# Performance work log

Hardware: AMD Instinct MI355X
Metric: run time of the kernel (lower is better)

Reference implementation:

```python
import jax, jax.numpy as jnp
import numpy as np

VOCAB, EMB, OUT = 32000, 1024, 10
B, S = 64, 512

def setup_inputs() -> dict:
    key = jax.random.key(0)
    k1, k2, k3, k4, k5, k6, k7 = jax.random.split(key, 7)
    x = jax.random.randint(k1, (B, S), 0, VOCAB)
    label = jax.random.randint(k2, (B,), 0, OUT)
    emb_table = jax.random.normal(k3, (VOCAB, EMB), dtype=jnp.float32) * 0.02
    W = jax.random.normal(k4, (EMB, EMB), dtype=jnp.float32) / np.sqrt(EMB)
    b = jax.random.normal(k5, (EMB,), dtype=jnp.float32) * 0.01
    Wc = jax.random.normal(k6, (OUT, EMB), dtype=jnp.float32) / np.sqrt(EMB)
    bc = jax.random.normal(k7, (OUT,), dtype=jnp.float32) * 0.01
    return {"x": x, "label": label, "emb_table": emb_table, "W": W, "b": b, "Wc": Wc, "bc": bc}

def reference(x, label, emb_table, W, b, Wc, bc):
    # embedding lookup: (B, S, EMB)
    emb = emb_table[x]
    # affine recurrence h_i = W @ (h_{i-1} + x_i) + b, h_{-1} = 0
    def step(h, xi):
        h = (h + xi) @ W.T + b  # (B, EMB)
        return h, h
    h0 = jnp.zeros((emb.shape[0], emb.shape[2]), dtype=emb.dtype)
    _, hs = jax.lax.scan(step, h0, jnp.swapaxes(emb, 0, 1))  # hs: (S, B, EMB)
    result = jnp.swapaxes(hs, 0, 1)  # (B, S, EMB)
    pred = result @ Wc.T + bc  # (B, S, OUT)
    pred_mean = jnp.mean(pred, axis=1)  # (B, OUT)
    # cross entropy (mean reduction)
    logp = jax.nn.log_softmax(pred_mean, axis=-1)
    loss = -jnp.mean(jnp.take_along_axis(logp, label[:, None], axis=-1))
    return loss
```

## Files before the change

### kernel.cpp

```cpp
#include <hip/hip_runtime.h>

#define OFF_C    0L
#define OFF_CS   11272192L
#define OFF_WP   11354112L
#define OFF_BS   11436032L
#define OFF_PRED 11446272L
#define OFF_PART 11446912L
#define OFF_U16  11774592L
#define UQAH 0L
#define UQAL 1048576L
#define UQATH 2097152L
#define UQATL 3145728L
#define UQBH 4194304L
#define UQBL 5242880L
#define UQBTH 6291456L
#define UQBTL 7340032L
#define URH  8388608L
#define CSA  1409024L
#define CSB  2621440L

typedef unsigned short u16;
typedef unsigned int u32;
typedef u16 us8 __attribute__((ext_vector_type(8)));
typedef short s8v __attribute__((ext_vector_type(8)));
typedef float f4v __attribute__((ext_vector_type(4)));

__device__ __forceinline__ u16 f2b(float f) {
    u32 u = __float_as_uint(f);
    return (u16)((u + 0x7fffu + ((u >> 16) & 1u)) >> 16);
}
__device__ __forceinline__ float b2f(u16 h) {
    return __uint_as_float((u32)h << 16);
}

__global__ __launch_bounds__(256) void split_w(
    const float* __restrict__ W, u16* __restrict__ Qh, u16* __restrict__ Ql,
    u16* __restrict__ QTh, u16* __restrict__ QTl)
{
    __shared__ u32 T[64][65];
    const int tid = threadIdx.x;
    const int r = tid >> 2, c0 = (tid & 3) << 4;
    alignas(16) u16 h[16], l[16];
    const size_t src = (size_t)(blockIdx.y * 64 + r) * 1024 + blockIdx.x * 64 + c0;
    #pragma unroll
    for (int q = 0; q < 4; q++) {
        float4 v = *(const float4*)(W + src + q * 4);
        float vv[4] = {v.x, v.y, v.z, v.w};
        #pragma unroll
        for (int i = 0; i < 4; i++) {
            u16 hh = f2b(vv[i]);
            u16 ll = f2b(vv[i] - b2f(hh));
            h[q * 4 + i] = hh; l[q * 4 + i] = ll;
            T[c0 + q * 4 + i][r] = ((u32)ll << 16) | hh;
        }
    }
    *(us8*)(Qh + src) = *(const us8*)&h[0];
    *(us8*)(Qh + src + 8) = *(const us8*)&h[8];
    *(us8*)(Ql + src) = *(const us8*)&l[0];
    *(us8*)(Ql + src + 8) = *(const us8*)&l[8];
    __syncthreads();
    alignas(16) u16 th[16], tl[16];
    #pragma unroll
    for (int i = 0; i < 16; i++) {
        u32 v = T[r][c0 + i];
        th[i] = (u16)(v & 0xffffu); tl[i] = (u16)(v >> 16);
    }
    const size_t dst = (size_t)(blockIdx.x * 64 + r) * 1024 + blockIdx.y * 64 + c0;
    *(us8*)(QTh + dst) = *(const us8*)&th[0];
    *(us8*)(QTh + dst + 8) = *(const us8*)&th[8];
    *(us8*)(QTl + dst) = *(const us8*)&tl[0];
    *(us8*)(QTl + dst + 8) = *(const us8*)&tl[8];
}

__global__ __launch_bounds__(256) void thin_d0(
    const float* __restrict__ Wc, const float* __restrict__ W, float* __restrict__ pbuf)
{
    const int o = blockIdx.x >> 2;
    const int d = ((blockIdx.x & 3) << 8) + threadIdx.x;
    const int k0 = blockIdx.y << 7;
    float acc = 0.f;
    #pragma unroll 8
    for (int k = k0; k < k0 + 128; k++)
        acc = fmaf(Wc[o * 1024 + k], W[(size_t)k * 1024 + d], acc);
    pbuf[(size_t)blockIdx.y * 10240 + o * 1024 + d] = acc;
}

__global__ __launch_bounds__(256) void d0_fin(
    const float* __restrict__ pbuf, u16* __restrict__ Rh)
{
    const int od = blockIdx.x * 256 + threadIdx.x;
    float v = 0.f;
    #pragma unroll
    for (int z = 0; z < 8; z++) v += pbuf[(size_t)z * 10240 + od];
    Rh[od] = f2b(v);
}

__global__ __launch_bounds__(256) void gemm_mfma(
    const u16* __restrict__ Ah_g, const u16* __restrict__ Al_g,
    const u16* __restrict__ Rh_g,
    const u16* __restrict__ BTh_g, const u16* __restrict__ BTl_g,
    float* __restrict__ C, int a1M, int a2M, int kc, long cS)
{
    const int M = a1M + a2M;
    __shared__ alignas(16) u16 Ash[4][129][8], Asl[4][129][8];
    __shared__ alignas(16) u16 Bsh[4][129][8], Bsl[4][129][8];
    const int tid = threadIdx.x;
    const int bn = blockIdx.x << 7, bm = blockIdx.y << 7;
    const int kstart = blockIdx.z * kc, kend = kstart + kc;
    const int lane = tid & 63, wid = tid >> 6;
    const int wm = (wid & 1) << 6, wn = (wid >> 1) << 6;
    const int lrow = lane & 15, kq = lane >> 4;
    const int srow = tid >> 1;
    const int skq = (tid & 1) << 1;
    const int sk = skq << 3;

    const u16* pBh = BTh_g + (size_t)(bn + srow) * 1024;
    const u16* pBl = BTl_g + (size_t)(bn + srow) * 1024;

    f4v acc[4][4];
    #pragma unroll
    for (int i = 0; i < 4; i++)
        #pragma unroll
        for (int j = 0; j < 4; j++) acc[i][j] = 0.f;

    if (bm < a1M) {
        const u16* pAh = Ah_g + (size_t)(bm + srow) * 1024;
        const u16* pAl = Al_g + (size_t)(bm + srow) * 1024;
        us8 ah0, ah1, al0, al1, bh0, bh1, bl0, bl1;
        auto loadstep = [&](int k) {
            ah0 = *(const us8*)(pAh + k + sk); ah1 = *(const us8*)(pAh + k + sk + 8);
            al0 = *(const us8*)(pAl + k + sk); al1 = *(const us8*)(pAl + k + sk + 8);
            bh0 = *(const us8*)(pBh + k + sk); bh1 = *(const us8*)(pBh + k + sk + 8);
            bl0 = *(const us8*)(pBl + k + sk); bl1 = *(const us8*)(pBl + k + sk + 8);
        };
        loadstep(kstart);
        for (int k0 = kstart; k0 < kend; k0 += 32) {
            *(us8*)&Ash[skq][srow][0] = ah0;
            *(us8*)&Ash[skq + 1][srow][0] = ah1;
            *(us8*)&Asl[skq][srow][0] = al0;
            *(us8*)&Asl[skq + 1][srow][0] = al1;
            *(us8*)&Bsh[skq][srow][0] = bh0;
            *(us8*)&Bsh[skq + 1][srow][0] = bh1;
            *(us8*)&Bsl[skq][srow][0] = bl0;
            *(us8*)&Bsl[skq + 1][srow][0] = bl1;
            __syncthreads();
            if (k0 + 32 < kend) loadstep(k0 + 32);
            s8v afh[4], afl[4], bfh[4], bfl[4];
            #pragma unroll
            for (int i = 0; i < 4; i++) {
                afh[i] = *(const s8v*)&Ash[kq][wm + (i << 4) + lrow][0];
                afl[i] = *(const s8v*)&Asl[kq][wm + (i << 4) + lrow][0];
                bfh[i] = *(const s8v*)&Bsh[kq][wn + (i << 4) + lrow][0];
                bfl[i] = *(const s8v*)&Bsl[kq][wn + (i << 4) + lrow][0];
            }
            #pragma unroll
            for (int mi = 0; mi < 4; mi++)
                #pragma unroll
                for (int ni = 0; ni < 4; ni++) {
                    acc[mi][ni] = __builtin_amdgcn_mfma_f32_16x16x32_bf16(
                        afh[mi], bfh[ni], acc[mi][ni], 0, 0, 0);
                    acc[mi][ni] = __builtin_amdgcn_mfma_f32_16x16x32_bf16(
                        afl[mi], bfh[ni], acc[mi][ni], 0, 0, 0);
                    acc[mi][ni] = __builtin_amdgcn_mfma_f32_16x16x32_bf16(
                        afh[mi], bfl[ni], acc[mi][ni], 0, 0, 0);
                }
            __syncthreads();
        }
    } else {
        const int rr = bm + srow - a1M;
        const bool aval = (rr < a2M);
        const u16* pAh = Rh_g + (size_t)(aval ? rr : 0) * 1024;
        us8 ah0, ah1, bh0, bh1, bl0, bl1;
        auto loadstep = [&](int k) {
            if (aval) {
                ah0 = *(const us8*)(pAh + k + sk); ah1 = *(const us8*)(pAh + k + sk + 8);
            } else { ah0 = 0; ah1 = 0; }
            bh0 = *(const us8*)(pBh + k + sk); bh1 = *(const us8*)(pBh + k + sk + 8);
            bl0 = *(const us8*)(pBl + k + sk); bl1 = *(const us8*)(pBl + k + sk + 8);
        };
        loadstep(kstart);
        for (int k0 = kstart; k0 < kend; k0 += 32) {
            *(us8*)&Ash[skq][srow][0] = ah0;
            *(us8*)&Ash[skq + 1][srow][0] = ah1;
            *(us8*)&Bsh[skq][srow][0] = bh0;
            *(us8*)&Bsh[skq + 1][srow][0] = bh1;
            *(us8*)&Bsl[skq][srow][0] = bl0;
            *(us8*)&Bsl[skq + 1][srow][0] = bl1;
            __syncthreads();
            if (k0 + 32 < kend) loadstep(k0 + 32);
            s8v afh[4], bfh[4], bfl[4];
            #pragma unroll
            for (int i = 0; i < 4; i++) {
                afh[i] = *(const s8v*)&Ash[kq][wm + (i << 4) + lrow][0];
                bfh[i] = *(const s8v*)&Bsh[kq][wn + (i << 4) + lrow][0];
                bfl[i] = *(const s8v*)&Bsl[kq][wn + (i << 4) + lrow][0];
            }
            #pragma unroll
            for (int mi = 0; mi < 4; mi++)
                #pragma unroll
                for (int ni = 0; ni < 4; ni++) {
                    acc[mi][ni] = __builtin_amdgcn_mfma_f32_16x16x32_bf16(
                        afh[mi], bfh[ni], acc[mi][ni], 0, 0, 0);
                    acc[mi][ni] = __builtin_amdgcn_mfma_f32_16x16x32_bf16(
                        afh[mi], bfl[ni], acc[mi][ni], 0, 0, 0);
                }
            __syncthreads();
        }
    }
    float* Cz = C + (size_t)blockIdx.z * cS;
    #pragma unroll
    for (int mi = 0; mi < 4; mi++)
        #pragma unroll
        for (int i = 0; i < 4; i++) {
            const int gr = bm + wm + (mi << 4) + (kq << 2) + i;
            if (gr >= M) continue;
            #pragma unroll
            for (int ni = 0; ni < 4; ni++)
                Cz[(size_t)gr * 1024 + bn + wn + (ni << 4) + lrow] = acc[mi][ni][i];
        }
}

__global__ __launch_bounds__(256) void combine(
    const float* __restrict__ C, int zsplit, long cS, int a1M, int a2M, int M,
    u16* __restrict__ Qh, u16* __restrict__ Ql,
    u16* __restrict__ QTh, u16* __restrict__ QTl,
    u16* __restrict__ Rh)
{
    __shared__ u32 T[64][65];
    const int tid = threadIdx.x;
    const int r = tid >> 2, c0 = (tid & 3) << 4;
    const int row0 = blockIdx.y << 6, col0 = blockIdx.x << 6;
    const int gr = row0 + r;
    const bool isQ = (row0 < a1M);
    alignas(16) u16 h[16], l[16];
    #pragma unroll
    for (int q = 0; q < 4; q++) {
        float4 v = make_float4(0.f, 0.f, 0.f, 0.f);
        if (gr < M) {
            const float* p = C + (size_t)gr * 1024 + col0 + c0 + q * 4;
            v = *(const float4*)p;
            for (int z = 1; z < zsplit; z++) {
                float4 t = *(const float4*)(p + (size_t)z * cS);
                v.x += t.x; v.y += t.y; v.z += t.z; v.w += t.w;
            }
        }
        float vv[4] = {v.x, v.y, v.z, v.w};
        #pragma unroll
        for (int i = 0; i < 4; i++) {
            u16 hh = f2b(vv[i]);
            u16 ll = f2b(vv[i] - b2f(hh));
            h[q * 4 + i] = hh; l[q * 4 + i] = ll;
            if (isQ) T[c0 + q * 4 + i][r] = ((u32)ll << 16) | hh;
        }
    }
    if (isQ) {
        const size_t dst = (size_t)gr * 1024 + col0 + c0;
        *(us8*)(Qh + dst) = *(const us8*)&h[0];
        *(us8*)(Qh + dst + 8) = *(const us8*)&h[8];
        *(us8*)(Ql + dst) = *(const us8*)&l[0];
        *(us8*)(Ql + dst + 8) = *(const us8*)&l[8];
        __syncthreads();
        alignas(16) u16 th[16], tl[16];
        #pragma unroll
        for (int i = 0; i < 16; i++) {
            u32 v = T[r][c0 + i];
            th[i] = (u16)(v & 0xffffu); tl[i] = (u16)(v >> 16);
        }
        const size_t dt = (size_t)(col0 + r) * 1024 + row0 + c0;
        *(us8*)(QTh + dt) = *(const us8*)&th[0];
        *(us8*)(QTh + dt + 8) = *(const us8*)&th[8];
        *(us8*)(QTl + dt) = *(const us8*)&tl[0];
        *(us8*)(QTl + dt + 8) = *(const us8*)&tl[8];
    } else if (gr < M) {
        const size_t dst = (size_t)(gr - a1M + a2M) * 1024 + col0 + c0;
        *(us8*)(Rh + dst) = *(const us8*)&h[0];
        *(us8*)(Rh + dst + 8) = *(const us8*)&h[8];
    }
}

__global__ __launch_bounds__(256) void prefix_pass1(
    const u16* __restrict__ Rh, float* __restrict__ csum, float* __restrict__ wpart)
{
    const int od = blockIdx.x * 256 + threadIdx.x;
    const int c = blockIdx.y;
    const u16* ph = Rh + (size_t)(c * 64) * 10240 + od;
    float cs = 0.f, wsv = 0.f;
    #pragma unroll 4
    for (int i = 0; i < 64; i++) {
        float v = b2f(ph[(size_t)i * 10240]);
        cs += v;
        wsv += (float)(511 - (c * 64 + i)) * v;
    }
    csum[c * 10240 + od] = cs;
    wpart[c * 10240 + od] = wsv;
}

__global__ __launch_bounds__(256) void prefix_pass2(
    const u16* __restrict__ Rh, const float* __restrict__ csum, float* __restrict__ Acc)
{
    const int od = blockIdx.x * 256 + threadIdx.x;
    const int c = blockIdx.y;
    float run = 0.f;
    #pragma unroll
    for (int c2 = 0; c2 < 8; c2++) {
        float t = csum[c2 * 10240 + od];
        run += (c2 < c) ? t : 0.f;
    }
    const u16* ph = Rh + (size_t)(c * 64) * 10240 + od;
    float* pa = Acc + (size_t)(c * 64) * 10240 + od;
    #pragma unroll 4
    for (int i = 0; i < 64; i++) {
        run += b2f(ph[(size_t)i * 10240]);
        pa[(size_t)i * 10240] = run;
    }
}

__global__ __launch_bounds__(256) void bsum_k(
    const float* __restrict__ wpart, const float* __restrict__ Wc, float* __restrict__ bsum)
{
    const int od = blockIdx.x * 256 + threadIdx.x;
    float s = 512.f * Wc[od];
    #pragma unroll
    for (int c = 0; c < 8; c++) s += wpart[c * 10240 + od];
    bsum[od] = s;
}

__global__ __launch_bounds__(256) void contract_k(
    const float* __restrict__ Acc, const int* __restrict__ x,
    const float* __restrict__ emb, float* __restrict__ part)
{
    __shared__ float As[10240];
    const int tid = threadIdx.x;
    const int j = blockIdx.x;
    const int w = tid >> 6, lane = tid & 63;
    const float4* emb4 = (const float4*)emb;
    float4* As4 = (float4*)As;
    const float4* Ap = (const float4*)(Acc + (size_t)(511 - j) * 10240);

    int i0 = x[((w << 2) + 0) * 512 + j], i1 = x[((w << 2) + 1) * 512 + j];
    int i2 = x[((w << 2) + 2) * 512 + j], i3 = x[((w << 2) + 3) * 512 + j];
    float4 e0[4], e1[4], e2[4], e3[4];
    #pragma unroll
    for (int c = 0; c < 4; c++) {
        e0[c] = emb4[(size_t)i0 * 256 + (c << 6) + lane];
        e1[c] = emb4[(size_t)i1 * 256 + (c << 6) + lane];
        e2[c] = emb4[(size_t)i2 * 256 + (c << 6) + lane];
        e3[c] = emb4[(size_t)i3 * 256 + (c << 6) + lane];
    }
    #pragma unroll
    for (int i = 0; i < 10; i++) As4[tid + (i << 8)] = Ap[tid + (i << 8)];
    __syncthreads();

    for (int chunk = 0; chunk < 4; chunk++) {
        float p0[10], p1[10], p2[10], p3[10];
        #pragma unroll
        for (int o = 0; o < 10; o++) {
            float s0 = 0.f, s1 = 0.f, s2 = 0.f, s3 = 0.f;
            #pragma unroll
            for (int c = 0; c < 4; c++) {
                float4 a = As4[(o << 8) + (c << 6) + lane];
                s0 = fmaf(a.x, e0[c].x, s0); s0 = fmaf(a.y, e0[c].y, s0);
                s0 = fmaf(a.z, e0[c].z, s0); s0 = fmaf(a.w, e0[c].w, s0);
                s1 = fmaf(a.x, e1[c].x, s1); s1 = fmaf(a.y, e1[c].y, s1);
                s1 = fmaf(a.z, e1[c].z, s1); s1 = fmaf(a.w, e1[c].w, s1);
                s2 = fmaf(a.x, e2[c].x, s2); s2 = fmaf(a.y, e2[c].y, s2);
                s2 = fmaf(a.z, e2[c].z, s2); s2 = fmaf(a.w, e2[c].w, s2);
                s3 = fmaf(a.x, e3[c].x, s3); s3 = fmaf(a.y, e3[c].y, s3);
                s3 = fmaf(a.z, e3[c].z, s3); s3 = fmaf(a.w, e3[c].w, s3);
            }
            p0[o] = s0; p1[o] = s1; p2[o] = s2; p3[o] = s3;
        }
        if (chunk < 3) {
            const int bn = ((chunk + 1) << 4) + (w << 2);
            i0 = x[(bn + 0) * 512 + j]; i1 = x[(bn + 1) * 512 + j];
            i2 = x[(bn + 2) * 512 + j]; i3 = x[(bn + 3) * 512 + j];
            #pragma unroll
            for (int c = 0; c < 4; c++) {
                e0[c] = emb4[(size_t)i0 * 256 + (c << 6) + lane];
                e1[c] = emb4[(size_t)i1 * 256 + (c << 6) + lane];
                e2[c] = emb4[(size_t)i2 * 256 + (c << 6) + lane];
                e3[c] = emb4[(size_t)i3 * 256 + (c << 6) + lane];
            }
        }
        #pragma unroll
        for (int o = 0; o < 10; o++) {
            #pragma unroll
            for (int off = 32; off; off >>= 1) {
                p0[o] += __shfl_down(p0[o], off);
                p1[o] += __shfl_down(p1[o], off);
                p2[o] += __shfl_down(p2[o], off);
                p3[o] += __shfl_down(p3[o], off);
            }
        }
        if (lane == 0) {
            const int bbase = (chunk << 4) + (w << 2);
            float* pp = part + (size_t)j * 640 + bbase * 10;
            #pragma unroll
            for (int o = 0; o < 10; o++) {
                pp[o] = p0[o]; pp[10 + o] = p1[o];
                pp[20 + o] = p2[o]; pp[30 + o] = p3[o];
            }
        }
    }
}

__global__ __launch_bounds__(256) void reduce_part(
    const float* __restrict__ part, float* __restrict__ pred)
{
    const int gid = blockIdx.x * 256 + threadIdx.x;
    const int out = gid >> 4, s = gid & 15;
    float p = 0.f;
    #pragma unroll 8
    for (int t = 0; t < 32; t++) p += part[(size_t)(s + (t << 4)) * 640 + out];
    for (int off = 8; off; off >>= 1) p += __shfl_down(p, off, 16);
    if (s == 0) pred[out] = p;
}

__global__ __launch_bounds__(640) void finalize_k(
    const float* __restrict__ pred, const float* __restrict__ bsum,
    const float* __restrict__ bvec, const float* __restrict__ bc,
    const int* __restrict__ label, float* __restrict__ out)
{
    __shared__ float biasv[10];
    const int tid = threadIdx.x;
    {
        int o = tid >> 6, lane = tid & 63;
        float s = 0.f;
        for (int k = lane; k < 1024; k += 64) s = fmaf(bsum[o * 1024 + k], bvec[k], s);
        for (int off = 32; off; off >>= 1) s += __shfl_down(s, off, 64);
        if (lane == 0) biasv[o] = s;
    }
    __syncthreads();
    if (tid < 64) {
        int b = tid, lab = label[b];
        float v[10], mx = -1e30f;
        #pragma unroll
        for (int o = 0; o < 10; o++) {
            v[o] = (pred[b * 10 + o] + biasv[o]) * (1.f / 512.f) + bc[o];
            mx = fmaxf(mx, v[o]);
        }
        float se = 0.f, vl = 0.f;
        #pragma unroll
        for (int o = 0; o < 10; o++) {
            se += __expf(v[o] - mx);
            if (o == lab) vl = v[o];
        }
        float myloss = (mx + __logf(se)) - vl;
        for (int off = 32; off; off >>= 1) myloss += __shfl_down(myloss, off, 64);
        if (tid == 0) out[0] = myloss * (1.f / 64.f);
    }
}

extern "C" void kernel_launch(void* const* d_in, const int* in_sizes, int n_in,
                              void* d_out, int out_size, void* d_ws, size_t ws_size,
                              hipStream_t stream) {
    const int*   x     = (const int*)d_in[0];
    const int*   label = (const int*)d_in[1];
    const float* emb   = (const float*)d_in[2];
    const float* W     = (const float*)d_in[3];
    const float* bvec  = (const float*)d_in[4];
    const float* Wc    = (const float*)d_in[5];
    const float* bc    = (const float*)d_in[6];
    float* ws    = (float*)d_ws;
    float* C     = ws + OFF_C;
    float* Acc   = ws + OFF_C;
    float* csum  = ws + OFF_CS;
    float* wpart = ws + OFF_WP;
    float* bsum  = ws + OFF_BS;
    float* pred  = ws + OFF_PRED;
    float* part  = ws + OFF_PART;
    u16*   ub    = (u16*)(ws + OFF_U16);
    u16* RH = ub + URH;
    u16* qin[4]  = {ub + UQAH, ub + UQAL, ub + UQATH, ub + UQATL};
    u16* qout[4] = {ub + UQBH, ub + UQBL, ub + UQBTH, ub + UQBTL};
    float* out   = (float*)d_out;

    split_w<<<dim3(16, 16), 256, 0, stream>>>(W, qin[0], qin[1], qin[2], qin[3]);
    thin_d0<<<dim3(40, 8), 256, 0, stream>>>(Wc, W, C);
    d0_fin<<<40, 256, 0, stream>>>(C, RH);

    int a2M = 10;
    for (int k = 2; k <= 10; k++) {
        const int a1M = (k < 10) ? 1024 : 0;
        const int M = a1M + a2M;
        const int zs = (M <= 1376) ? 4 : 2;
        const long cS = (zs == 4) ? CSA : CSB;
        const int kc = 1024 / zs;
        dim3 g(8, (M + 127) / 128, zs);
        gemm_mfma<<<g, 256, 0, stream>>>(qin[0], qin[1], RH, qin[2], qin[3],
                                         C, a1M, a2M, kc, cS);
        combine<<<dim3(16, (M + 63) / 64), 256, 0, stream>>>(
            C, zs, cS, a1M, a2M, M,
            qout[0], qout[1], qout[2], qout[3], RH);
        for (int i = 0; i < 4; i++) { u16* t = qin[i]; qin[i] = qout[i]; qout[i] = t; }
        a2M <<= 1;
    }

    prefix_pass1<<<dim3(40, 8), 256, 0, stream>>>(RH, csum, wpart);
    prefix_pass2<<<dim3(40, 8), 256, 0, stream>>>(RH, csum, Acc);
    bsum_k<<<40, 256, 0, stream>>>(wpart, Wc, bsum);
    contract_k<<<512, 256, 0, stream>>>(Acc, x, emb, part);
    reduce_part<<<40, 256, 0, stream>>>(part, pred);
    finalize_k<<<1, 640, 0, stream>>>(pred, bsum, bvec, bc, label, out);
}
```

Before: 504.3 us.

## Fuse split-K combine into GEMM via last-block atomic counter; merge small kernels

The separate combine kernel after each split-K GEMM is removed. The last K-split block for each output tile, found with an atomic counter and thread fences, now sums the partials and writes the bf16 hi/lo and transposed outputs itself. thin_d0 and d0_fin are merged into one shared-memory kernel, and bsum_k is folded into finalize_k. This cuts about a dozen kernel launches and their gaps, at the cost of a memset, atomics, and serialized combine work in a few tail blocks.

```diff
diff --git a/kernel.cpp b/kernel.cpp
--- a/kernel.cpp
+++ b/kernel.cpp
@@ -3,10 +3,10 @@
 #define OFF_C    0L
 #define OFF_CS   11272192L
 #define OFF_WP   11354112L
-#define OFF_BS   11436032L
 #define OFF_PRED 11446272L
 #define OFF_PART 11446912L
 #define OFF_U16  11774592L
+#define OFF_CNT  18590336L
 #define UQAH 0L
 #define UQAL 1048576L
 #define UQATH 2097152L
@@ -72,38 +72,53 @@
     *(us8*)(QTl + dst + 8) = *(const us8*)&tl[8];
 }
 
-__global__ __launch_bounds__(256) void thin_d0(
-    const float* __restrict__ Wc, const float* __restrict__ W, float* __restrict__ pbuf)
-{
-    const int o = blockIdx.x >> 2;
-    const int d = ((blockIdx.x & 3) << 8) + threadIdx.x;
-    const int k0 = blockIdx.y << 7;
-    float acc = 0.f;
-    #pragma unroll 8
-    for (int k = k0; k < k0 + 128; k++)
-        acc = fmaf(Wc[o * 1024 + k], W[(size_t)k * 1024 + d], acc);
-    pbuf[(size_t)blockIdx.y * 10240 + o * 1024 + d] = acc;
-}
-
-__global__ __launch_bounds__(256) void d0_fin(
-    const float* __restrict__ pbuf, u16* __restrict__ Rh)
-{
-    const int od = blockIdx.x * 256 + threadIdx.x;
-    float v = 0.f;
-    #pragma unroll
-    for (int z = 0; z < 8; z++) v += pbuf[(size_t)z * 10240 + od];
-    Rh[od] = f2b(v);
+__global__ __launch_bounds__(256) void d0_k(
+    const float* __restrict__ Wc, const float* __restrict__ W, u16* __restrict__ Rh)
+{
+    __shared__ float WcS[10240];
+    __shared__ float red[8][332];
+    const int tid = threadIdx.x;
+    const int d = tid & 31, kz = tid >> 5;
+    const int dbase = blockIdx.x << 5;
+    for (int i = tid; i < 2560; i += 256)
+        ((float4*)WcS)[i] = ((const float4*)Wc)[i];
+    __syncthreads();
+    float acc[10] = {};
+    const int k0 = kz << 7;
+    for (int k = 0; k < 128; k++) {
+        float w = W[(size_t)(k0 + k) * 1024 + dbase + d];
+        #pragma unroll
+        for (int o = 0; o < 10; o++)
+            acc[o] = fmaf(WcS[o * 1024 + k0 + k], w, acc[o]);
+    }
+    #pragma unroll
+    for (int o = 0; o < 10; o++) red[kz][o * 32 + d] = acc[o];
+    __syncthreads();
+    for (int t = tid; t < 320; t += 256) {
+        float s = 0.f;
+        #pragma unroll
+        for (int z = 0; z < 8; z++) s += red[z][t];
+        Rh[(size_t)(t >> 5) * 1024 + dbase + (t & 31)] = f2b(s);
+    }
 }
 
 __global__ __launch_bounds__(256) void gemm_mfma(
     const u16* __restrict__ Ah_g, const u16* __restrict__ Al_g,
     const u16* __restrict__ Rh_g,
     const u16* __restrict__ BTh_g, const u16* __restrict__ BTl_g,
-    float* __restrict__ C, int a1M, int a2M, int kc, long cS)
+    float* __restrict__ C, int a1M, int a2M, int kc, long cS, int zs,
+    int* __restrict__ cnt,
+    u16* __restrict__ Qh, u16* __restrict__ Ql,
+    u16* __restrict__ QTh, u16* __restrict__ QTl,
+    u16* __restrict__ Rh_out)
 {
     const int M = a1M + a2M;
-    __shared__ alignas(16) u16 Ash[4][129][8], Asl[4][129][8];
-    __shared__ alignas(16) u16 Bsh[4][129][8], Bsl[4][129][8];
+    __shared__ alignas(16) char smem[33024];
+    u16 (*Ash)[129][8] = (u16(*)[129][8])(smem);
+    u16 (*Asl)[129][8] = (u16(*)[129][8])(smem + 8256);
+    u16 (*Bsh)[129][8] = (u16(*)[129][8])(smem + 16512);
+    u16 (*Bsl)[129][8] = (u16(*)[129][8])(smem + 24768);
+    __shared__ int isLastS;
     const int tid = threadIdx.x;
     const int bn = blockIdx.x << 7, bm = blockIdx.y << 7;
     const int kstart = blockIdx.z * kc, kend = kstart + kc;
@@ -218,63 +233,68 @@
             for (int ni = 0; ni < 4; ni++)
                 Cz[(size_t)gr * 1024 + bn + wn + (ni << 4) + lrow] = acc[mi][ni][i];
         }
-}
-
-__global__ __launch_bounds__(256) void combine(
-    const float* __restrict__ C, int zsplit, long cS, int a1M, int a2M, int M,
-    u16* __restrict__ Qh, u16* __restrict__ Ql,
-    u16* __restrict__ QTh, u16* __restrict__ QTl,
-    u16* __restrict__ Rh)
-{
-    __shared__ u32 T[64][65];
-    const int tid = threadIdx.x;
-    const int r = tid >> 2, c0 = (tid & 3) << 4;
-    const int row0 = blockIdx.y << 6, col0 = blockIdx.x << 6;
-    const int gr = row0 + r;
-    const bool isQ = (row0 < a1M);
-    alignas(16) u16 h[16], l[16];
-    #pragma unroll
-    for (int q = 0; q < 4; q++) {
-        float4 v = make_float4(0.f, 0.f, 0.f, 0.f);
-        if (gr < M) {
-            const float* p = C + (size_t)gr * 1024 + col0 + c0 + q * 4;
-            v = *(const float4*)p;
-            for (int z = 1; z < zsplit; z++) {
-                float4 t = *(const float4*)(p + (size_t)z * cS);
-                v.x += t.x; v.y += t.y; v.z += t.z; v.w += t.w;
-            }
-        }
-        float vv[4] = {v.x, v.y, v.z, v.w};
-        #pragma unroll
-        for (int i = 0; i < 4; i++) {
-            u16 hh = f2b(vv[i]);
-            u16 ll = f2b(vv[i] - b2f(hh));
-            h[q * 4 + i] = hh; l[q * 4 + i] = ll;
-            if (isQ) T[c0 + q * 4 + i][r] = ((u32)ll << 16) | hh;
-        }
-    }
-    if (isQ) {
-        const size_t dst = (size_t)gr * 1024 + col0 + c0;
-        *(us8*)(Qh + dst) = *(const us8*)&h[0];
-        *(us8*)(Qh + dst + 8) = *(const us8*)&h[8];
-        *(us8*)(Ql + dst) = *(const us8*)&l[0];
-        *(us8*)(Ql + dst + 8) = *(const us8*)&l[8];
-        __syncthreads();
-        alignas(16) u16 th[16], tl[16];
-        #pragma unroll
-        for (int i = 0; i < 16; i++) {
-            u32 v = T[r][c0 + i];
-            th[i] = (u16)(v & 0xffffu); tl[i] = (u16)(v >> 16);
-        }
-        const size_t dt = (size_t)(col0 + r) * 1024 + row0 + c0;
-        *(us8*)(QTh + dt) = *(const us8*)&th[0];
-        *(us8*)(QTh + dt + 8) = *(const us8*)&th[8];
-        *(us8*)(QTl + dt) = *(const us8*)&tl[0];
-        *(us8*)(QTl + dt + 8) = *(const us8*)&tl[8];
-    } else if (gr < M) {
-        const size_t dst = (size_t)(gr - a1M + a2M) * 1024 + col0 + c0;
-        *(us8*)(Rh + dst) = *(const us8*)&h[0];
-        *(us8*)(Rh + dst + 8) = *(const us8*)&h[8];
+    __syncthreads();
+    if (tid == 0) {
+        __threadfence();
+        const int tile = (int)(blockIdx.y * gridDim.x + blockIdx.x);
+        int old = atomicAdd(&cnt[tile], 1);
+        int last = (old == zs - 1) ? 1 : 0;
+        if (last) __threadfence();
+        isLastS = last;
+    }
+    __syncthreads();
+    if (!isLastS) return;
+    u32 (*T)[65] = (u32(*)[65])(smem);
+    const bool isQ = (bm < a1M);
+    const int r = tid >> 2, cq0 = (tid & 3) << 4;
+    for (int sub = 0; sub < 4; sub++) {
+        const int r0 = bm + ((sub >> 1) << 6), c0 = bn + ((sub & 1) << 6);
+        const int gr = r0 + r;
+        alignas(16) u16 h[16], l[16];
+        #pragma unroll
+        for (int q = 0; q < 4; q++) {
+            float4 v = make_float4(0.f, 0.f, 0.f, 0.f);
+            if (gr < M) {
+                const float* p = C + (size_t)gr * 1024 + c0 + cq0 + q * 4;
+                v = *(const float4*)p;
+                for (int z = 1; z < zs; z++) {
+                    float4 t2 = *(const float4*)(p + (size_t)z * cS);
+                    v.x += t2.x; v.y += t2.y; v.z += t2.z; v.w += t2.w;
+                }
+            }
+            float vv[4] = {v.x, v.y, v.z, v.w};
+            #pragma unroll
+            for (int i = 0; i < 4; i++) {
+                u16 hh = f2b(vv[i]);
+                u16 ll = f2b(vv[i] - b2f(hh));
+                h[q * 4 + i] = hh; l[q * 4 + i] = ll;
+                if (isQ) T[cq0 + q * 4 + i][r] = ((u32)ll << 16) | hh;
+            }
+        }
+        if (isQ) {
+            const size_t dst = (size_t)gr * 1024 + c0 + cq0;
+            *(us8*)(Qh + dst) = *(const us8*)&h[0];
+            *(us8*)(Qh + dst + 8) = *(const us8*)&h[8];
+            *(us8*)(Ql + dst) = *(const us8*)&l[0];
+            *(us8*)(Ql + dst + 8) = *(const us8*)&l[8];
+            __syncthreads();
+            alignas(16) u16 th[16], tl[16];
+            #pragma unroll
+            for (int i = 0; i < 16; i++) {
+                u32 v = T[r][cq0 + i];
+                th[i] = (u16)(v & 0xffffu); tl[i] = (u16)(v >> 16);
+            }
+            const size_t dt = (size_t)(c0 + r) * 1024 + r0 + cq0;
+            *(us8*)(QTh + dt) = *(const us8*)&th[0];
+            *(us8*)(QTh + dt + 8) = *(const us8*)&th[8];
+            *(us8*)(QTl + dt) = *(const us8*)&tl[0];
+            *(us8*)(QTl + dt + 8) = *(const us8*)&tl[8];
+            __syncthreads();
+        } else if (gr < M) {
+            const size_t dst = (size_t)(gr - a1M + a2M) * 1024 + c0 + cq0;
+            *(us8*)(Rh_out + dst) = *(const us8*)&h[0];
+            *(us8*)(Rh_out + dst + 8) = *(const us8*)&h[8];
+        }
     }
 }
 
@@ -313,16 +333,6 @@
         run += b2f(ph[(size_t)i * 10240]);
         pa[(size_t)i * 10240] = run;
     }
-}
-
-__global__ __launch_bounds__(256) void bsum_k(
-    const float* __restrict__ wpart, const float* __restrict__ Wc, float* __restrict__ bsum)
-{
-    const int od = blockIdx.x * 256 + threadIdx.x;
-    float s = 512.f * Wc[od];
-    #pragma unroll
-    for (int c = 0; c < 8; c++) s += wpart[c * 10240 + od];
-    bsum[od] = s;
 }
 
 __global__ __launch_bounds__(256) void contract_k(
@@ -417,16 +427,22 @@
 }
 
 __global__ __launch_bounds__(640) void finalize_k(
-    const float* __restrict__ pred, const float* __restrict__ bsum,
-    const float* __restrict__ bvec, const float* __restrict__ bc,
-    const int* __restrict__ label, float* __restrict__ out)
+    const float* __restrict__ pred, const float* __restrict__ wpart,
+    const float* __restrict__ Wc, const float* __restrict__ bvec,
+    const float* __restrict__ bc, const int* __restrict__ label,
+    float* __restrict__ out)
 {
     __shared__ float biasv[10];
     const int tid = threadIdx.x;
     {
         int o = tid >> 6, lane = tid & 63;
         float s = 0.f;
-        for (int k = lane; k < 1024; k += 64) s = fmaf(bsum[o * 1024 + k], bvec[k], s);
+        for (int k = lane; k < 1024; k += 64) {
+            float wsum = 512.f * Wc[o * 1024 + k];
+            #pragma unroll
+            for (int c = 0; c < 8; c++) wsum += wpart[c * 10240 + o * 1024 + k];
+            s = fmaf(wsum, bvec[k], s);
+        }
         for (int off = 32; off; off >>= 1) s += __shfl_down(s, off, 64);
         if (lane == 0) biasv[o] = s;
     }
@@ -466,18 +482,18 @@
     float* Acc   = ws + OFF_C;
     float* csum  = ws + OFF_CS;
     float* wpart = ws + OFF_WP;
-    float* bsum  = ws + OFF_BS;
     float* pred  = ws + OFF_PRED;
     float* part  = ws + OFF_PART;
+    int*   cnt   = (int*)(ws + OFF_CNT);
     u16*   ub    = (u16*)(ws + OFF_U16);
     u16* RH = ub + URH;
     u16* qin[4]  = {ub + UQAH, ub + UQAL, ub + UQATH, ub + UQATL};
     u16* qout[4] = {ub + UQBH, ub + UQBL, ub + UQBTH, ub + UQBTL};
     float* out   = (float*)d_out;
 
+    hipMemsetAsync(cnt, 0, 9 * 160 * sizeof(int), stream);
     split_w<<<dim3(16, 16), 256, 0, stream>>>(W, qin[0], qin[1], qin[2], qin[3]);
-    thin_d0<<<dim3(40, 8), 256, 0, stream>>>(Wc, W, C);
-    d0_fin<<<40, 256, 0, stream>>>(C, RH);
+    d0_k<<<32, 256, 0, stream>>>(Wc, W, RH);
 
     int a2M = 10;
     for (int k = 2; k <= 10; k++) {
@@ -487,10 +503,9 @@
         const long cS = (zs == 4) ? CSA : CSB;
         const int kc = 1024 / zs;
         dim3 g(8, (M + 127) / 128, zs);
-        gemm_mfma<<<g, 256, 0, stream>>>(qin[0], qin[1], RH, qin[2], qin[3],
-                                         C, a1M, a2M, kc, cS);
-        combine<<<dim3(16, (M + 63) / 64), 256, 0, stream>>>(
-            C, zs, cS, a1M, a2M, M,
+        gemm_mfma<<<g, 256, 0, stream>>>(
+            qin[0], qin[1], RH, qin[2], qin[3],
+            C, a1M, a2M, kc, cS, zs, cnt + (size_t)(k - 2) * 160,
             qout[0], qout[1], qout[2], qout[3], RH);
         for (int i = 0; i < 4; i++) { u16* t = qin[i]; qin[i] = qout[i]; qout[i] = t; }
         a2M <<= 1;
@@ -498,8 +513,7 @@
 
     prefix_pass1<<<dim3(40, 8), 256, 0, stream>>>(RH, csum, wpart);
     prefix_pass2<<<dim3(40, 8), 256, 0, stream>>>(RH, csum, Acc);
-    bsum_k<<<40, 256, 0, stream>>>(wpart, Wc, bsum);
     contract_k<<<512, 256, 0, stream>>>(Acc, x, emb, part);
     reduce_part<<<40, 256, 0, stream>>>(part, pred);
-    finalize_k<<<1, 640, 0, stream>>>(pred, bsum, bvec, bc, label, out);
-}
+    finalize_k<<<1, 640, 0, stream>>>(pred, wpart, Wc, bvec, bc, label, out);
+}
```

Result: slower. 691.3 us (+37.1%).
